# Performance work log

Measured on AMD Instinct MI355X. Metric: run time of the kernel, lower is better.

## Reference

```python
import jax, jax.numpy as jnp
import numpy as np

K = 16      # num neighbors
EPS = 1e-5  # std epsilon


def _masked_stats(x, mask):
    # x: [B,P,F]; mask: [B,P] with True = padded/invalid point
    valid = (~mask)[:, :, None].astype(x.dtype)
    cnt = jnp.maximum(valid.sum(1, keepdims=True), 1.0)
    mean = (x * valid).sum(1, keepdims=True) / cnt
    var = (((x - mean) ** 2) * valid).sum(1, keepdims=True) / cnt
    return mean, jnp.sqrt(var)


def setup_inputs() -> dict:
    key = jax.random.key(0)
    k0, k1, k2 = jax.random.split(key, 3)
    B, P, D, d_model = 16, 2048, 16, 512
    in_dim = D * K * 2  # 512
    x = jax.random.normal(k0, (B, P, D), jnp.float32)
    features = jax.random.randint(k1, (B, D), 0, 2).astype(jnp.float32)
    attn_mask = jnp.zeros((B, P), dtype=bool)
    W = jax.random.normal(k2, (2 * d_model, in_dim), jnp.float32) / np.sqrt(in_dim)
    b = jnp.zeros((2 * d_model,), jnp.float32)
    return {"x": x, "features": features, "attn_mask": attn_mask, "W": W, "b": b}


def reference(x, features, attn_mask, W, b):
    B, P, D = x.shape
    feat = features[:, None, :] > 0.1                 # [B,1,D]
    x_crd = jnp.where(feat, 0.0, x)                   # coordinate columns
    x_ftr = jnp.where(feat, x, 0.0)                   # objective/feature columns
    xc = jnp.concatenate([x_crd, x_ftr], axis=-1)     # [B,P,2D]
    mean, std = _masked_stats(xc, attn_mask)
    xn = jnp.clip((xc - mean) / (std + EPS), -10.0, 10.0)
    # pairwise L2 distances on raw coordinates (torch.cdist, p=2)
    sq = (x_crd ** 2).sum(-1)                         # [B,P]
    d2 = sq[:, :, None] + sq[:, None, :] - 2.0 * jnp.einsum('bpd,bqd->bpq', x_crd, x_crd)
    dist = jnp.sqrt(jnp.maximum(d2, 0.0))             # [B,P,P]
    dist = jnp.where(attn_mask[:, None, :], jnp.inf, dist)  # never pick padded points
    _, idx = jax.lax.top_k(-dist, K)                  # k smallest -> idx [B,P,K]; idx[...,0] is self
    knn = jax.vmap(lambda xb, ib: xb[ib])(xn, idx)    # gather neighbors [B,P,K,2D]
    center = knn[:, :, :1]                            # self features
    knn = jnp.concatenate([center, knn[:, :, 1:] - center], axis=2)  # project_local: neighbors rel. to self
    out = knn.reshape(B, P, K * 2 * D)                # [B,P,num_df*k*2]
    h = out @ W.T + b                                 # Linear -> [B,P,2*d_model]
    a, g = jnp.split(h, 2, axis=-1)
    return a * jax.nn.sigmoid(g)                      # GLU (dropout = identity at eval)
```

## Files before the change

kernel.cpp:

```cpp
#include <hip/hip_runtime.h>
#include <stdint.h>
#include <stddef.h>

#define EPS 1e-5f
#define EPS_M 4e-3f
#define CAP 96

typedef __attribute__((ext_vector_type(8))) short bf16x8;
typedef __attribute__((ext_vector_type(4))) float f32x4;
typedef _Float16 f16x8 __attribute__((ext_vector_type(8)));
typedef unsigned long long u64;

__device__ __forceinline__ unsigned short f2bf(float f){
  unsigned u = __float_as_uint(f);
  u = (u + 0x7FFFu + ((u >> 16) & 1u)) >> 16;
  return (unsigned short)u;
}

__device__ __forceinline__ void gload16(const void* g, void* l){
  __builtin_amdgcn_global_load_lds(
      (__attribute__((address_space(1))) const void*)g,
      (__attribute__((address_space(3))) void*)l, 16, 0, 0);
}

__global__ __launch_bounds__(256) void k_stats(const float* __restrict__ x,
                                               float* __restrict__ meanA,
                                               float* __restrict__ stdA){
  int bd = blockIdx.x;
  int b = bd >> 4, d = bd & 15;
  const float* xb = x + (size_t)b * 2048 * 16 + d;
  float s = 0.f, s2 = 0.f;
  for (int p = threadIdx.x; p < 2048; p += 256){
    float v = xb[(size_t)p * 16];
    s += v; s2 = fmaf(v, v, s2);
  }
  __shared__ float rs[256], rq[256];
  rs[threadIdx.x] = s; rq[threadIdx.x] = s2;
  __syncthreads();
  for (int off = 128; off > 0; off >>= 1){
    if (threadIdx.x < off){
      rs[threadIdx.x] += rs[threadIdx.x + off];
      rq[threadIdx.x] += rq[threadIdx.x + off];
    }
    __syncthreads();
  }
  if (threadIdx.x == 0){
    float mean = rs[0] * (1.f / 2048.f);
    float var  = rq[0] * (1.f / 2048.f) - mean * mean;
    var = fmaxf(var, 0.f);
    meanA[bd] = mean;
    stdA[bd]  = sqrtf(var);
  }
}

__global__ __launch_bounds__(256) void k_norm(const float* __restrict__ x,
    const float* __restrict__ features, const float* __restrict__ meanA,
    const float* __restrict__ stdA, float* __restrict__ xn,
    float* __restrict__ xcrd, float* __restrict__ sqA,
    _Float16* __restrict__ xh){
  int m = blockIdx.x * 256 + threadIdx.x;
  int b = m >> 11;
  const float* xp = x + (size_t)m * 16;
  float on[32];
  float sq = 0.f;
  #pragma unroll
  for (int d = 0; d < 16; d++){
    float v = xp[d];
    bool f = features[b * 16 + d] > 0.1f;
    float nrm = (v - meanA[b * 16 + d]) / (stdA[b * 16 + d] + EPS);
    nrm = fminf(fmaxf(nrm, -10.f), 10.f);
    float crd = f ? 0.f : v;
    xcrd[(size_t)m * 16 + d] = crd;
    sq = fmaf(crd, crd, sq);
    _Float16 h1 = (_Float16)crd;
    float h2f = crd - (float)h1;
    xh[(size_t)m * 32 + d]      = h1;
    xh[(size_t)m * 32 + 16 + d] = (_Float16)h2f;
    on[d]      = f ? 0.f : nrm;
    on[16 + d] = f ? nrm : 0.f;
  }
  sqA[m] = sq;
  #pragma unroll
  for (int d = 0; d < 32; d++) xn[(size_t)m * 32 + d] = on[d];
}

__global__ __launch_bounds__(256) void k_scan(const _Float16* __restrict__ xh,
    const float* __restrict__ sqA, unsigned short* __restrict__ survG,
    unsigned int* __restrict__ cntG){
  int bid = blockIdx.x;
  int qs = bid & 3, pt = (bid >> 2) & 31, b = bid >> 7;
  int p0 = pt * 64, q0 = qs * 512;
  int tid = threadIdx.x, w = tid >> 6, l = tid & 63;
  int l15 = l & 15, g = l >> 4;
  const _Float16* xhb = xh + (size_t)b * 2048 * 32;
  const float*    sqb = sqA + (size_t)b * 2048;

  f16x8 hz;
  #pragma unroll
  for (int j = 0; j < 8; j++) hz[j] = (_Float16)0.f;

  int p_mine = p0 + w * 16 + l15;
  int jb = g & 1;
  f16x8 B1 = *(const f16x8*)(xhb + (size_t)p_mine * 32 + jb * 8);
  f16x8 B2 = *(const f16x8*)(xhb + (size_t)p_mine * 32 + 16 + jb * 8);
  if (g >= 2) B2 = hz;
  float sqp = sqb[p_mine];

  float d0r = __builtin_inff(), d1r = __builtin_inff();
  float d2r = __builtin_inff(), d3r = __builtin_inff();

  const _Float16* arow = xhb + (size_t)(q0 + l15) * 32 + g * 8;

  #pragma unroll 4
  for (int T = 0; T < 32; T++){
    f16x8 A1 = *(const f16x8*)(arow + (size_t)T * 16 * 32);
    f32x4 acc = {0.f, 0.f, 0.f, 0.f};
    acc = __builtin_amdgcn_mfma_f32_16x16x32_f16(A1, B1, acc, 0, 0, 0);
    acc = __builtin_amdgcn_mfma_f32_16x16x32_f16(A1, B2, acc, 0, 0, 0);
    f32x4 sqq = *(const f32x4*)(sqb + q0 + T * 16 + g * 4);
    #pragma unroll
    for (int r = 0; r < 4; r++){
      float dd = fmaf(-2.f, acc[r], sqp + sqq[r]);
      d3r = __builtin_amdgcn_fmed3f(dd, d2r, d3r);
      d2r = __builtin_amdgcn_fmed3f(dd, d1r, d2r);
      d1r = __builtin_amdgcn_fmed3f(dd, d0r, d1r);
      d0r = fminf(d0r, dd);
    }
  }
  float t4 = d3r;
  t4 = fmaxf(t4, __shfl_xor(t4, 16));
  t4 = fmaxf(t4, __shfl_xor(t4, 32));
  float tlim = t4 + EPS_M;
  unsigned long long gmask = 0x0001000100010001ULL << l15;
  int cnt = 0;
  size_t key = ((size_t)(b * 2048 + p_mine)) * 4 + qs;
  unsigned short* mysurv = survG + key * CAP;
  #pragma unroll 4
  for (int T = 0; T < 32; T++){
    f16x8 A1 = *(const f16x8*)(arow + (size_t)T * 16 * 32);
    f32x4 acc = {0.f, 0.f, 0.f, 0.f};
    acc = __builtin_amdgcn_mfma_f32_16x16x32_f16(A1, B1, acc, 0, 0, 0);
    acc = __builtin_amdgcn_mfma_f32_16x16x32_f16(A1, B2, acc, 0, 0, 0);
    f32x4 sqq = *(const f32x4*)(sqb + q0 + T * 16 + g * 4);
    #pragma unroll
    for (int r = 0; r < 4; r++){
      float dd = fmaf(-2.f, acc[r], sqp + sqq[r]);
      bool pass = dd <= tlim;
      unsigned long long mp = __ballot(pass) & gmask;
      int ofs = __builtin_amdgcn_mbcnt_hi((unsigned)(mp >> 32),
                __builtin_amdgcn_mbcnt_lo((unsigned)mp, 0));
      int slot = cnt + ofs;
      if (pass && slot < CAP)
        mysurv[slot] = (unsigned short)(q0 + T * 16 + g * 4 + r);
      cnt += (int)__popcll(mp);
    }
  }
  if (g == 0) cntG[key] = (unsigned int)cnt;
}

__global__ __launch_bounds__(256, 1) void k_rerank(const unsigned short* __restrict__ survG,
    const unsigned int* __restrict__ cntG, const float* __restrict__ xcrd,
    const float* __restrict__ sqA, int* __restrict__ kidx){
  __shared__ u64 K_s[16][16][16];
  __shared__ u64 K2[4][16][16];
  int tid = threadIdx.x;
  int p_l = tid & 15, lid = tid >> 4;
  int qs = lid & 3, h = lid >> 2;
  int b = blockIdx.x >> 7, pt = blockIdx.x & 127;
  int p = pt * 16 + p_l;
  int q0 = qs * 512;
  const float* sqb = sqA + (size_t)b * 2048;
  size_t key = ((size_t)(b * 2048 + p)) * 4 + qs;
  int n = (int)cntG[key];
  bool fb = (n > CAP);
  int total = fb ? 512 : n;
  const unsigned short* sv = survG + key * CAP;

  const float4* xpg = (const float4*)(xcrd + ((size_t)b * 2048 + p) * 16);
  float xp[16];
  #pragma unroll
  for (int i = 0; i < 4; i++){
    float4 v = xpg[i];
    xp[4*i+0] = v.x; xp[4*i+1] = v.y; xp[4*i+2] = v.z; xp[4*i+3] = v.w;
  }
  float sqpp = sqb[p];
  u64 d[16];
  #pragma unroll
  for (int i = 0; i < 16; i++) d[i] = ~0ULL;
  for (int si = h; si < total; si += 4){
    int q = fb ? (q0 + si) : (int)sv[si];
    const float4* xqg = (const float4*)(xcrd + ((size_t)b * 2048 + q) * 16);
    float4 v0 = xqg[0], v1 = xqg[1], v2 = xqg[2], v3 = xqg[3];
    float a0 = fmaf(xp[0],  v0.x, fmaf(xp[1],  v0.y, fmaf(xp[2],  v0.z, xp[3]  * v0.w)));
    float a1 = fmaf(xp[4],  v1.x, fmaf(xp[5],  v1.y, fmaf(xp[6],  v1.z, xp[7]  * v1.w)));
    float a2 = fmaf(xp[8],  v2.x, fmaf(xp[9],  v2.y, fmaf(xp[10], v2.z, xp[11] * v2.w)));
    float a3 = fmaf(xp[12], v3.x, fmaf(xp[13], v3.y, fmaf(xp[14], v3.z, xp[15] * v3.w)));
    float dot = (a0 + a1) + (a2 + a3);
    float dd = fmaf(-2.f, dot, sqpp + sqb[q]);
    dd = fmaxf(dd, 0.f);
    u64 k64 = ((u64)__float_as_uint(dd) << 32) | (unsigned)q;
    #pragma unroll
    for (int j = 15; j >= 1; j--){
      bool cj  = k64 < d[j];
      bool cjm = k64 < d[j - 1];
      d[j] = cj ? (cjm ? d[j - 1] : k64) : d[j];
    }
    d[0] = (k64 < d[0]) ? k64 : d[0];
  }
  #pragma unroll
  for (int j = 0; j < 16; j++) K_s[lid][j][p_l] = d[j];
  __syncthreads();
  if (tid < 64){
    int p2 = tid & 15, q2 = tid >> 4;
    int base = q2 * 4;
    int j0 = 0, j1 = 0, j2 = 0, j3 = 0;
    #pragma unroll
    for (int r = 0; r < 16; r++){
      u64 k0 = K_s[base + 0][j0][p2];
      u64 k1 = K_s[base + 1][j1][p2];
      u64 k2 = K_s[base + 2][j2][p2];
      u64 k3 = K_s[base + 3][j3][p2];
      u64 best = k0; int ws = 0;
      if (k1 < best){ best = k1; ws = 1; }
      if (k2 < best){ best = k2; ws = 2; }
      if (k3 < best){ best = k3; ws = 3; }
      K2[q2][r][p2] = best;
      j0 += (ws == 0); j1 += (ws == 1); j2 += (ws == 2); j3 += (ws == 3);
    }
  }
  __syncthreads();
  if (tid < 16){
    int p2 = tid;
    int j0 = 0, j1 = 0, j2 = 0, j3 = 0;
    int* outp = kidx + ((size_t)(b * 2048 + pt * 16 + p2)) * 16;
    #pragma unroll
    for (int r = 0; r < 16; r++){
      u64 k0 = K2[0][j0][p2];
      u64 k1 = K2[1][j1][p2];
      u64 k2 = K2[2][j2][p2];
      u64 k3 = K2[3][j3][p2];
      u64 best = k0; int ws = 0;
      if (k1 < best){ best = k1; ws = 1; }
      if (k2 < best){ best = k2; ws = 2; }
      if (k3 < best){ best = k3; ws = 3; }
      outp[r] = (int)(unsigned)(best & 0xFFFFFFFFu);
      j0 += (ws == 0); j1 += (ws == 1); j2 += (ws == 2); j3 += (ws == 3);
    }
  }
}

__global__ __launch_bounds__(256) void k_build_a(const float* __restrict__ xn,
    const int* __restrict__ knnIdx, unsigned short* __restrict__ A){
  int m = blockIdx.x * 4 + (threadIdx.x >> 6);
  int lane = threadIdx.x & 63;
  int k = lane >> 2, cg = lane & 3;
  int b = m >> 11;
  int i0 = knnIdx[m * 16];
  int ik = knnIdx[m * 16 + k];
  const float* v0 = xn + ((size_t)b * 2048 + i0) * 32 + cg * 8;
  const float* vk = xn + ((size_t)b * 2048 + ik) * 32 + cg * 8;
  bf16x8 pk;
  #pragma unroll
  for (int c = 0; c < 8; c++){
    float z = v0[c];
    float o = (k == 0) ? z : (vk[c] - z);
    pk[c] = (short)f2bf(o);
  }
  *(bf16x8*)(A + (size_t)m * 512 + k * 32 + cg * 8) = pk;
}

__global__ __launch_bounds__(256) void k_wconv(const float* __restrict__ W,
                                               unsigned short* __restrict__ Wb){
  int i = blockIdx.x * 256 + threadIdx.x;
  float4 v = ((const float4*)W)[i];
  ushort4 o;
  o.x = f2bf(v.x); o.y = f2bf(v.y); o.z = f2bf(v.z); o.w = f2bf(v.w);
  ((ushort4*)Wb)[i] = o;
}

__global__ __launch_bounds__(256) void k_gemm(const unsigned short* __restrict__ A,
    const unsigned short* __restrict__ Wb, const float* __restrict__ bias,
    float* __restrict__ out){
  __shared__ unsigned short As[2][128 * 32];
  __shared__ unsigned short Ws[2][128 * 32];
  int blk = blockIdx.x;
  int bn = (blk >> 3) & 7;
  int bm = (blk & 7) | ((blk >> 6) << 3);
  int m0 = bm * 128, n0 = bn * 64;
  int tid = threadIdx.x, wid = tid >> 6, lane = tid & 63;
  int wr = wid >> 1, wc = wid & 1;
  f32x4 zero = {0.f, 0.f, 0.f, 0.f};
  f32x4 acc1[4][2], acc2[4][2];
  #pragma unroll
  for (int i = 0; i < 4; i++){
    #pragma unroll
    for (int jj = 0; jj < 2; jj++){ acc1[i][jj] = zero; acc2[i][jj] = zero; }
  }
  int l15 = lane & 15, hi = lane >> 4;

  #define GSTAGE(buf, kt) do {                                               \
    int k0_ = (kt) * 32;                                                     \
    _Pragma("unroll")                                                        \
    for (int i_ = 0; i_ < 2; i_++){                                          \
      int id_ = tid + i_ * 256;                                              \
      int row_ = id_ >> 2, c_ = id_ & 3;                                     \
      int cs_ = c_ ^ ((row_ >> 1) & 3);                                      \
      gload16(A + (size_t)(m0 + row_) * 512 + k0_ + cs_ * 8,                 \
              (char*)As[buf] + id_ * 16);                                    \
      int wrow_ = n0 + (row_ & 63) + ((row_ >> 6) << 9);                     \
      gload16(Wb + (size_t)wrow_ * 512 + k0_ + cs_ * 8,                      \
              (char*)Ws[buf] + id_ * 16);                                    \
    }                                                                        \
  } while (0)

  GSTAGE(0, 0);
  __syncthreads();
  int cur = 0;
  for (int kt = 0; kt < 16; kt++){
    if (kt < 15) GSTAGE(cur ^ 1, kt + 1);
    bf16x8 af[4], b1f[2], b2f[2];
    #pragma unroll
    for (int i = 0; i < 4; i++){
      int r = wr * 64 + i * 16 + l15;
      af[i] = *(const bf16x8*)&As[cur][r * 32 + (hi ^ ((r >> 1) & 3)) * 8];
    }
    #pragma unroll
    for (int jj = 0; jj < 2; jj++){
      int r = wc * 32 + jj * 16 + l15;
      b1f[jj] = *(const bf16x8*)&Ws[cur][r * 32 + (hi ^ ((r >> 1) & 3)) * 8];
      int r2 = 64 + r;
      b2f[jj] = *(const bf16x8*)&Ws[cur][r2 * 32 + (hi ^ ((r2 >> 1) & 3)) * 8];
    }
    #pragma unroll
    for (int i = 0; i < 4; i++){
      #pragma unroll
      for (int jj = 0; jj < 2; jj++){
        acc1[i][jj] = __builtin_amdgcn_mfma_f32_16x16x32_bf16(af[i], b1f[jj], acc1[i][jj], 0, 0, 0);
        acc2[i][jj] = __builtin_amdgcn_mfma_f32_16x16x32_bf16(af[i], b2f[jj], acc2[i][jj], 0, 0, 0);
      }
    }
    __syncthreads();
    cur ^= 1;
  }
  #pragma unroll
  for (int i = 0; i < 4; i++){
    int row = m0 + wr * 64 + i * 16 + (lane >> 4) * 4;
    #pragma unroll
    for (int jj = 0; jj < 2; jj++){
      int col = n0 + wc * 32 + jj * 16 + l15;
      float b1v = bias[col], b2v = bias[512 + col];
      #pragma unroll
      for (int r = 0; r < 4; r++){
        float av = acc1[i][jj][r] + b1v;
        float gv = acc2[i][jj][r] + b2v;
        float s = 1.f / (1.f + __expf(-gv));
        out[(size_t)(row + r) * 512 + col] = av * s;
      }
    }
  }
}

extern "C" void kernel_launch(void* const* d_in, const int* in_sizes, int n_in,
                              void* d_out, int out_size, void* d_ws, size_t ws_size,
                              hipStream_t stream){
  const float* x        = (const float*)d_in[0];
  const float* features = (const float*)d_in[1];
  const float* W        = (const float*)d_in[3];
  const float* bias     = (const float*)d_in[4];
  float* out = (float*)d_out;
  char* ws = (char*)d_ws;

  float* meanA = (float*)(ws + 0);
  float* stdA  = (float*)(ws + 1024);
  float* xn    = (float*)(ws + 4096);
  float* xcrd  = (float*)(ws + 4198400);
  float* sqA   = (float*)(ws + 6295552);
  int*   kidx  = (int*)  (ws + 6426624);
  unsigned short* Wbf = (unsigned short*)(ws + 8523776);
  _Float16* xh = (_Float16*)(ws + 9572352);
  unsigned int*   cntG  = (unsigned int*)  (ws + 11669504);
  unsigned short* survG = (unsigned short*)(ws + 12193792);
  unsigned short* Abf   = (unsigned short*)(ws + 9572352);

  k_stats  <<<256,  256, 0, stream>>>(x, meanA, stdA);
  k_norm   <<<128,  256, 0, stream>>>(x, features, meanA, stdA, xn, xcrd, sqA, xh);
  k_scan   <<<2048, 256, 0, stream>>>(xh, sqA, survG, cntG);
  k_rerank <<<2048, 256, 0, stream>>>(survG, cntG, xcrd, sqA, kidx);
  k_build_a<<<8192, 256, 0, stream>>>(xn, kidx, Abf);
  k_wconv  <<<512,  256, 0, stream>>>(W, Wbf);
  k_gemm   <<<2048, 256, 0, stream>>>(Abf, Wbf, bias, out);
}
```

Baseline: 205.1 us.

## Fuse neighbor gather into rerank kernel and shrink survivor capacity

Measured after the change: 284.3 us. +38.6%, slower.

```diff
diff --git a/kernel.cpp b/kernel.cpp
--- a/kernel.cpp
+++ b/kernel.cpp
@@ -4,7 +4,7 @@
 
 #define EPS 1e-5f
 #define EPS_M 4e-3f
-#define CAP 96
+#define CAP 48
 
 typedef __attribute__((ext_vector_type(8))) short bf16x8;
 typedef __attribute__((ext_vector_type(4))) float f32x4;
@@ -160,9 +160,11 @@
 
 __global__ __launch_bounds__(256, 1) void k_rerank(const unsigned short* __restrict__ survG,
     const unsigned int* __restrict__ cntG, const float* __restrict__ xcrd,
-    const float* __restrict__ sqA, int* __restrict__ kidx){
+    const float* __restrict__ sqA, const float* __restrict__ xn,
+    unsigned short* __restrict__ Abf){
   __shared__ u64 K_s[16][16][16];
   __shared__ u64 K2[4][16][16];
+  __shared__ unsigned short fin_s[16][16];
   int tid = threadIdx.x;
   int p_l = tid & 15, lid = tid >> 4;
   int qs = lid & 3, h = lid >> 2;
@@ -232,7 +234,6 @@
   if (tid < 16){
     int p2 = tid;
     int j0 = 0, j1 = 0, j2 = 0, j3 = 0;
-    int* outp = kidx + ((size_t)(b * 2048 + pt * 16 + p2)) * 16;
     #pragma unroll
     for (int r = 0; r < 16; r++){
       u64 k0 = K2[0][j0][p2];
@@ -243,30 +244,31 @@
       if (k1 < best){ best = k1; ws = 1; }
       if (k2 < best){ best = k2; ws = 2; }
       if (k3 < best){ best = k3; ws = 3; }
-      outp[r] = (int)(unsigned)(best & 0xFFFFFFFFu);
+      fin_s[p2][r] = (unsigned short)(best & 0xFFFFu);
       j0 += (ws == 0); j1 += (ws == 1); j2 += (ws == 2); j3 += (ws == 3);
     }
   }
-}
-
-__global__ __launch_bounds__(256) void k_build_a(const float* __restrict__ xn,
-    const int* __restrict__ knnIdx, unsigned short* __restrict__ A){
-  int m = blockIdx.x * 4 + (threadIdx.x >> 6);
-  int lane = threadIdx.x & 63;
-  int k = lane >> 2, cg = lane & 3;
-  int b = m >> 11;
-  int i0 = knnIdx[m * 16];
-  int ik = knnIdx[m * 16 + k];
-  const float* v0 = xn + ((size_t)b * 2048 + i0) * 32 + cg * 8;
-  const float* vk = xn + ((size_t)b * 2048 + ik) * 32 + cg * 8;
-  bf16x8 pk;
-  #pragma unroll
-  for (int c = 0; c < 8; c++){
-    float z = v0[c];
-    float o = (k == 0) ? z : (vk[c] - z);
-    pk[c] = (short)f2bf(o);
-  }
-  *(bf16x8*)(A + (size_t)m * 512 + k * 32 + cg * 8) = pk;
+  __syncthreads();
+  {
+    int p2 = tid >> 4, k = tid & 15;
+    int i0 = fin_s[p2][0];
+    int ik = fin_s[p2][k];
+    const float4* v0 = (const float4*)(xn + ((size_t)b * 2048 + i0) * 32);
+    const float4* vk = (const float4*)(xn + ((size_t)b * 2048 + ik) * 32);
+    size_t m = (size_t)b * 2048 + pt * 16 + p2;
+    unsigned short* dst = Abf + m * 512 + k * 32;
+    #pragma unroll
+    for (int c4 = 0; c4 < 8; c4++){
+      float4 z = v0[c4];
+      float4 w = vk[c4];
+      ushort4 o;
+      o.x = f2bf((k == 0) ? z.x : (w.x - z.x));
+      o.y = f2bf((k == 0) ? z.y : (w.y - z.y));
+      o.z = f2bf((k == 0) ? z.z : (w.z - z.z));
+      o.w = f2bf((k == 0) ? z.w : (w.w - z.w));
+      *(ushort4*)(dst + c4 * 4) = o;
+    }
+  }
 }
 
 __global__ __launch_bounds__(256) void k_wconv(const float* __restrict__ W,
@@ -375,18 +377,16 @@
   float* xn    = (float*)(ws + 4096);
   float* xcrd  = (float*)(ws + 4198400);
   float* sqA   = (float*)(ws + 6295552);
-  int*   kidx  = (int*)  (ws + 6426624);
-  unsigned short* Wbf = (unsigned short*)(ws + 8523776);
-  _Float16* xh = (_Float16*)(ws + 9572352);
-  unsigned int*   cntG  = (unsigned int*)  (ws + 11669504);
-  unsigned short* survG = (unsigned short*)(ws + 12193792);
-  unsigned short* Abf   = (unsigned short*)(ws + 9572352);
+  unsigned short* Wbf = (unsigned short*)(ws + 6426624);
+  _Float16* xh = (_Float16*)(ws + 7475200);
+  unsigned int*   cntG  = (unsigned int*)  (ws + 9572352);
+  unsigned short* survG = (unsigned short*)(ws + 10096640);
+  unsigned short* Abf   = (unsigned short*)(ws + 22679552);
 
   k_stats  <<<256,  256, 0, stream>>>(x, meanA, stdA);
   k_norm   <<<128,  256, 0, stream>>>(x, features, meanA, stdA, xn, xcrd, sqA, xh);
   k_scan   <<<2048, 256, 0, stream>>>(xh, sqA, survG, cntG);
-  k_rerank <<<2048, 256, 0, stream>>>(survG, cntG, xcrd, sqA, kidx);
-  k_build_a<<<8192, 256, 0, stream>>>(xn, kidx, Abf);
+  k_rerank <<<2048, 256, 0, stream>>>(survG, cntG, xcrd, sqA, xn, Abf);
   k_wconv  <<<512,  256, 0, stream>>>(W, Wbf);
   k_gemm   <<<2048, 256, 0, stream>>>(Abf, Wbf, bias, out);
 }
```
